# Kernel tuning notes

Measured on AMD Instinct MI355X. Metric: run time of the kernel, lower is better.

The kernel has to match this reference:

```python
import jax, jax.numpy as jnp
import numpy as np

N = 1024
IN_F = 256
OUT_F = 128
H = 4
NH = OUT_F // H  # 32
NEG_SLOPE = 0.2


def setup_inputs() -> dict:
    key = jax.random.key(0)
    k1, k2, k3, k4, k5 = jax.random.split(key, 5)
    h = jax.random.normal(k1, (N, IN_F), dtype=jnp.float32)
    adj_mat = jax.random.randint(k2, (N, N, 1), 0, 2, dtype=jnp.int32)
    s_in = 1.0 / np.sqrt(IN_F)
    s_nh = 1.0 / np.sqrt(NH)
    Wl = jax.random.uniform(k3, (H * NH, IN_F), jnp.float32, -s_in, s_in)
    Wr = jax.random.uniform(k4, (H * NH, IN_F), jnp.float32, -s_in, s_in)
    attn_w = jax.random.uniform(k5, (NH,), jnp.float32, -s_nh, s_nh)
    return {"h": h, "adj_mat": adj_mat, "Wl": Wl, "Wr": Wr, "attn_w": attn_w}


def reference(h, adj_mat, Wl, Wr, attn_w):
    n = h.shape[0]
    g_l = (h @ Wl.T).reshape(n, H, NH)  # [N,H,F]
    g_r = (h @ Wr.T).reshape(n, H, NH)  # [N,H,F]
    # g_sum[i, j] = g_l[j] + g_r[i]  (repeat / repeat_interleave semantics)
    g_sum = g_l[None, :, :, :] + g_r[:, None, :, :]  # [N,N,H,F]
    act = jnp.where(g_sum >= 0, g_sum, NEG_SLOPE * g_sum)
    e = jnp.einsum('ijhf,f->ijh', act, attn_w)  # [N,N,H]
    mask = adj_mat != 0  # [N,N,1] broadcasts over heads
    e = jnp.where(mask, e, -jnp.inf)
    a = jax.nn.softmax(e, axis=1)  # softmax over source nodes j
    h_prime = jnp.einsum('ijh,jhf->ihf', a, g_r).reshape(n, H * NH)
    # is_output_layer=False -> ELU (dropout is a no-op in eval)
    return jax.nn.elu(h_prime)
```

## Files before the change

kernel.cpp:

```cpp
#include <hip/hip_runtime.h>
#include <math.h>

#define NN 1024
#define IN_F 256
#define OUT_F 128
#define NHEADS 4
#define NHF 32
#define HPSTR 260

__global__ void __launch_bounds__(256) glr_gemm(const float* __restrict__ hmat,
                                                const float* __restrict__ Wl,
                                                const float* __restrict__ Wr,
                                                float* __restrict__ glh,
                                                float* __restrict__ grh) {
    __shared__ float hp[64 * HPSTR];
    const int tid = threadIdx.x;
    const int rg = blockIdx.x & 15;
    const int cs = blockIdx.x >> 4;

    const float4* __restrict__ hsrc = (const float4*)hmat + rg * (64 * 64);
#pragma unroll
    for (int i = 0; i < 16; ++i) {
        const int v = tid + i * 256;
        const int row = v >> 6, kq = v & 63;
        const float4 x = hsrc[v];
        *(float4*)(hp + row * HPSTR + kq * 4) = x;
    }
    __syncthreads();

    const int lane = tid & 63;
    const int wu = __builtin_amdgcn_readfirstlane(tid >> 6);
    const int c0 = cs * 16 + wu * 4;
    const float* __restrict__ wbase = (c0 < OUT_F) ? (Wl + c0 * IN_F)
                                                   : (Wr + (c0 - OUT_F) * IN_F);
    const float* __restrict__ hrow = hp + lane * HPSTR;

    float a0 = 0.f, a1 = 0.f, a2 = 0.f, a3 = 0.f;
#pragma unroll 4
    for (int kq = 0; kq < 64; ++kq) {
        const float4 hv = *(const float4*)(hrow + kq * 4);
        const float4 w0 = *(const float4*)(wbase + 0 * IN_F + kq * 4);
        const float4 w1 = *(const float4*)(wbase + 1 * IN_F + kq * 4);
        const float4 w2 = *(const float4*)(wbase + 2 * IN_F + kq * 4);
        const float4 w3 = *(const float4*)(wbase + 3 * IN_F + kq * 4);
        a0 = fmaf(hv.x, w0.x, fmaf(hv.y, w0.y, fmaf(hv.z, w0.z, fmaf(hv.w, w0.w, a0))));
        a1 = fmaf(hv.x, w1.x, fmaf(hv.y, w1.y, fmaf(hv.z, w1.z, fmaf(hv.w, w1.w, a1))));
        a2 = fmaf(hv.x, w2.x, fmaf(hv.y, w2.y, fmaf(hv.z, w2.z, fmaf(hv.w, w2.w, a2))));
        a3 = fmaf(hv.x, w3.x, fmaf(hv.y, w3.y, fmaf(hv.z, w3.z, fmaf(hv.w, w3.w, a3))));
    }

    const int row = rg * 64 + lane;
    const int cb = c0 & (OUT_F - 1);
    const int hh = cb >> 5;
    const int f  = cb & 31;
    float* __restrict__ dst = (c0 < OUT_F) ? glh : grh;
    float4 r; r.x = a0; r.y = a1; r.z = a2; r.w = a3;
    *(float4*)(dst + (hh * NN + row) * NHF + f) = r;
}

__global__ void __launch_bounds__(512) gat_main(const float* __restrict__ glh,
                                                const float* __restrict__ grh,
                                                const int* __restrict__ adj,
                                                const float* __restrict__ attn_w,
                                                float* __restrict__ out) {
    const int hh  = blockIdx.y;
    const int i0  = blockIdx.x * 8;
    const int tid = threadIdx.x;

    __shared__ float p_buf[8][1028];
    __shared__ float part[8][16][32];
    __shared__ float red[8][8];
    __shared__ float l_sh[8];

    float lpart[8];
#pragma unroll
    for (int ii = 0; ii < 8; ++ii) lpart[ii] = 0.f;

    for (int c = 0; c < 2; ++c) {
        const int j = (c << 9) + tid;
        const float* __restrict__ gp = glh + (hh * NN + j) * NHF;
        float gl[NHF];
#pragma unroll
        for (int f4 = 0; f4 < 8; ++f4) {
            const float4 v = *(const float4*)(gp + (f4 << 2));
            gl[4 * f4 + 0] = v.x; gl[4 * f4 + 1] = v.y;
            gl[4 * f4 + 2] = v.z; gl[4 * f4 + 3] = v.w;
        }
        float alpha = 0.f;
#pragma unroll
        for (int f = 0; f < NHF; ++f) alpha = fmaf(gl[f], attn_w[f], alpha);
        int adjv[8];
#pragma unroll
        for (int ii = 0; ii < 8; ++ii) adjv[ii] = adj[(i0 + ii) * NN + j];
#pragma unroll
        for (int ii = 0; ii < 8; ++ii) {
            const float* __restrict__ grp = grh + (hh * NN + i0 + ii) * NHF;
            float S0 = 0.f, S1 = 0.f;
#pragma unroll
            for (int f = 0; f < NHF; f += 2) {
                const float s0 = gl[f]     + grp[f];
                const float s1 = gl[f + 1] + grp[f + 1];
                S0 = fmaf(fabsf(s0), attn_w[f],     S0);
                S1 = fmaf(fabsf(s1), attn_w[f + 1], S1);
            }
            const float e = fmaf(0.4f, S0 + S1, 0.6f * alpha);
            const float p = adjv[ii] ? __expf(e) : 0.f;
            p_buf[ii][j] = p;
            lpart[ii] += p;
        }
    }

    const int lane = tid & 63, wv = tid >> 6;
#pragma unroll
    for (int ii = 0; ii < 8; ++ii) {
        float v = lpart[ii];
#pragma unroll
        for (int d = 32; d > 0; d >>= 1) v += __shfl_xor(v, d);
        if (lane == 0) red[ii][wv] = v;
    }
    __syncthreads();
    if (tid < 8) {
        float l = red[tid][0];
#pragma unroll
        for (int w = 1; w < 8; ++w) l += red[tid][w];
        l_sh[tid] = l;
    }
    __syncthreads();

    const int f  = tid & 31;
    const int js = tid >> 5;
    const float* __restrict__ gp = grh + hh * NN * NHF + f;
    float o[8];
#pragma unroll
    for (int ii = 0; ii < 8; ++ii) o[ii] = 0.f;
    const int jb = js << 6;
    for (int jj = 0; jj < 64; jj += 4) {
        const int j = jb + jj;
        const float g0 = gp[(j + 0) * NHF];
        const float g1 = gp[(j + 1) * NHF];
        const float g2 = gp[(j + 2) * NHF];
        const float g3 = gp[(j + 3) * NHF];
#pragma unroll
        for (int ii = 0; ii < 8; ++ii) {
            const float4 p4 = *(const float4*)&p_buf[ii][j];
            o[ii] = fmaf(p4.x, g0, fmaf(p4.y, g1, fmaf(p4.z, g2, fmaf(p4.w, g3, o[ii]))));
        }
    }
#pragma unroll
    for (int ii = 0; ii < 8; ++ii) part[ii][js][f] = o[ii];
    __syncthreads();

    if (tid < 256) {
        const int ii = tid >> 5, ff = tid & 31;
        float s = 0.f;
#pragma unroll
        for (int k = 0; k < 16; ++k) s += part[ii][k][ff];
        s /= l_sh[ii];
        const float r = (s > 0.f) ? s : (__expf(s) - 1.f);
        out[(i0 + ii) * OUT_F + hh * NHF + ff] = r;
    }
}

extern "C" void kernel_launch(void* const* d_in, const int* in_sizes, int n_in,
                              void* d_out, int out_size, void* d_ws, size_t ws_size,
                              hipStream_t stream) {
    const float* hmat = (const float*)d_in[0];
    const int*   adj  = (const int*)d_in[1];
    const float* Wl   = (const float*)d_in[2];
    const float* Wr   = (const float*)d_in[3];
    const float* aw   = (const float*)d_in[4];
    float* o          = (float*)d_out;

    float* glh = (float*)d_ws;
    float* grh = glh + NHEADS * NN * NHF;

    glr_gemm<<<dim3(256), dim3(256), 0, stream>>>(hmat, Wl, Wr, glh, grh);
    gat_main<<<dim3(NN / 8, NHEADS), dim3(512), 0, stream>>>(glh, grh, adj, aw, o);
}
```

Baseline: 101.0 us.

## Shrink row tiles and split GEMM K across lanes to raise parallelism

The projection GEMM now uses 16-row tiles with the K dimension split across four lane groups, reduced by shuffles, and launches four times as many blocks. The attention kernel processes 4 destination rows per block instead of 8, which doubles the grid. Its score loop now loads g_l in 16-wide halves to lower register pressure, and launch bounds are raised to encourage higher occupancy. The aim is to fill the GPU better and hide latency. The cost is that each adjacency and g_r column pass is amortized over fewer rows, so the repeated global loads per row grow.

After: 101.1 us. No clear change (+0.2%).

```diff
diff --git a/kernel.cpp b/kernel.cpp
--- a/kernel.cpp
+++ b/kernel.cpp
@@ -6,104 +6,122 @@
 #define OUT_F 128
 #define NHEADS 4
 #define NHF 32
+#define ITILE 4
 #define HPSTR 260
 
-__global__ void __launch_bounds__(256) glr_gemm(const float* __restrict__ hmat,
-                                                const float* __restrict__ Wl,
-                                                const float* __restrict__ Wr,
-                                                float* __restrict__ glh,
-                                                float* __restrict__ grh) {
-    __shared__ float hp[64 * HPSTR];
+__global__ void __launch_bounds__(256, 4) glr_gemm(const float* __restrict__ hmat,
+                                                   const float* __restrict__ Wl,
+                                                   const float* __restrict__ Wr,
+                                                   float* __restrict__ glh,
+                                                   float* __restrict__ grh) {
+    __shared__ float hp[16 * HPSTR];
     const int tid = threadIdx.x;
-    const int rg = blockIdx.x & 15;
-    const int cs = blockIdx.x >> 4;
-
-    const float4* __restrict__ hsrc = (const float4*)hmat + rg * (64 * 64);
-#pragma unroll
-    for (int i = 0; i < 16; ++i) {
+    const int rg = blockIdx.x & 63;
+    const int cs = blockIdx.x >> 6;
+
+    const float4* __restrict__ hsrc = (const float4*)hmat + rg * (16 * 64);
+#pragma unroll
+    for (int i = 0; i < 4; ++i) {
         const int v = tid + i * 256;
         const int row = v >> 6, kq = v & 63;
-        const float4 x = hsrc[v];
-        *(float4*)(hp + row * HPSTR + kq * 4) = x;
+        *(float4*)(hp + row * HPSTR + kq * 4) = hsrc[v];
     }
     __syncthreads();
 
     const int lane = tid & 63;
-    const int wu = __builtin_amdgcn_readfirstlane(tid >> 6);
-    const int c0 = cs * 16 + wu * 4;
-    const float* __restrict__ wbase = (c0 < OUT_F) ? (Wl + c0 * IN_F)
-                                                   : (Wr + (c0 - OUT_F) * IN_F);
-    const float* __restrict__ hrow = hp + lane * HPSTR;
+    const int row  = lane & 15;
+    const int kc   = lane >> 4;
+    const int wu   = __builtin_amdgcn_readfirstlane(tid >> 6);
+    const int c0   = cs * 16 + wu * 4;
+    const float* __restrict__ wb = (c0 < OUT_F) ? (Wl + c0 * IN_F)
+                                                : (Wr + (c0 - OUT_F) * IN_F);
+    const float* __restrict__ hrow = hp + row * HPSTR + kc * 64;
+    const float* __restrict__ wrow = wb + kc * 64;
 
     float a0 = 0.f, a1 = 0.f, a2 = 0.f, a3 = 0.f;
 #pragma unroll 4
-    for (int kq = 0; kq < 64; ++kq) {
-        const float4 hv = *(const float4*)(hrow + kq * 4);
-        const float4 w0 = *(const float4*)(wbase + 0 * IN_F + kq * 4);
-        const float4 w1 = *(const float4*)(wbase + 1 * IN_F + kq * 4);
-        const float4 w2 = *(const float4*)(wbase + 2 * IN_F + kq * 4);
-        const float4 w3 = *(const float4*)(wbase + 3 * IN_F + kq * 4);
+    for (int i = 0; i < 16; ++i) {
+        const float4 hv = *(const float4*)(hrow + i * 4);
+        const float4 w0 = *(const float4*)(wrow + 0 * IN_F + i * 4);
+        const float4 w1 = *(const float4*)(wrow + 1 * IN_F + i * 4);
+        const float4 w2 = *(const float4*)(wrow + 2 * IN_F + i * 4);
+        const float4 w3 = *(const float4*)(wrow + 3 * IN_F + i * 4);
         a0 = fmaf(hv.x, w0.x, fmaf(hv.y, w0.y, fmaf(hv.z, w0.z, fmaf(hv.w, w0.w, a0))));
         a1 = fmaf(hv.x, w1.x, fmaf(hv.y, w1.y, fmaf(hv.z, w1.z, fmaf(hv.w, w1.w, a1))));
         a2 = fmaf(hv.x, w2.x, fmaf(hv.y, w2.y, fmaf(hv.z, w2.z, fmaf(hv.w, w2.w, a2))));
         a3 = fmaf(hv.x, w3.x, fmaf(hv.y, w3.y, fmaf(hv.z, w3.z, fmaf(hv.w, w3.w, a3))));
     }
-
-    const int row = rg * 64 + lane;
-    const int cb = c0 & (OUT_F - 1);
-    const int hh = cb >> 5;
-    const int f  = cb & 31;
-    float* __restrict__ dst = (c0 < OUT_F) ? glh : grh;
-    float4 r; r.x = a0; r.y = a1; r.z = a2; r.w = a3;
-    *(float4*)(dst + (hh * NN + row) * NHF + f) = r;
+    a0 += __shfl_xor(a0, 16); a0 += __shfl_xor(a0, 32);
+    a1 += __shfl_xor(a1, 16); a1 += __shfl_xor(a1, 32);
+    a2 += __shfl_xor(a2, 16); a2 += __shfl_xor(a2, 32);
+    a3 += __shfl_xor(a3, 16); a3 += __shfl_xor(a3, 32);
+
+    if (kc == 0) {
+        const int cb = c0 & (OUT_F - 1);
+        const int hh = cb >> 5;
+        const int f  = cb & 31;
+        float* __restrict__ dst = (c0 < OUT_F) ? glh : grh;
+        float4 r; r.x = a0; r.y = a1; r.z = a2; r.w = a3;
+        *(float4*)(dst + (hh * NN + rg * 16 + row) * NHF + f) = r;
+    }
 }
 
-__global__ void __launch_bounds__(512) gat_main(const float* __restrict__ glh,
-                                                const float* __restrict__ grh,
-                                                const int* __restrict__ adj,
-                                                const float* __restrict__ attn_w,
-                                                float* __restrict__ out) {
+__global__ void __launch_bounds__(512, 8) gat_main(const float* __restrict__ glh,
+                                                   const float* __restrict__ grh,
+                                                   const int* __restrict__ adj,
+                                                   const float* __restrict__ attn_w,
+                                                   float* __restrict__ out) {
     const int hh  = blockIdx.y;
-    const int i0  = blockIdx.x * 8;
+    const int i0  = blockIdx.x * ITILE;
     const int tid = threadIdx.x;
 
-    __shared__ float p_buf[8][1028];
-    __shared__ float part[8][16][32];
-    __shared__ float red[8][8];
-    __shared__ float l_sh[8];
-
-    float lpart[8];
-#pragma unroll
-    for (int ii = 0; ii < 8; ++ii) lpart[ii] = 0.f;
-
+    __shared__ float p_buf[ITILE][1028];
+    __shared__ float part[ITILE][16][NHF];
+    __shared__ float red[ITILE][8];
+    __shared__ float l_sh[ITILE];
+
+    float lpart[ITILE];
+#pragma unroll
+    for (int ii = 0; ii < ITILE; ++ii) lpart[ii] = 0.f;
+
+#pragma unroll 1
     for (int c = 0; c < 2; ++c) {
         const int j = (c << 9) + tid;
         const float* __restrict__ gp = glh + (hh * NN + j) * NHF;
-        float gl[NHF];
-#pragma unroll
-        for (int f4 = 0; f4 < 8; ++f4) {
-            const float4 v = *(const float4*)(gp + (f4 << 2));
-            gl[4 * f4 + 0] = v.x; gl[4 * f4 + 1] = v.y;
-            gl[4 * f4 + 2] = v.z; gl[4 * f4 + 3] = v.w;
-        }
+        int adjv[ITILE];
+#pragma unroll
+        for (int ii = 0; ii < ITILE; ++ii) adjv[ii] = adj[(i0 + ii) * NN + j];
+
+        float S[ITILE];
+#pragma unroll
+        for (int ii = 0; ii < ITILE; ++ii) S[ii] = 0.f;
         float alpha = 0.f;
-#pragma unroll
-        for (int f = 0; f < NHF; ++f) alpha = fmaf(gl[f], attn_w[f], alpha);
-        int adjv[8];
-#pragma unroll
-        for (int ii = 0; ii < 8; ++ii) adjv[ii] = adj[(i0 + ii) * NN + j];
-#pragma unroll
-        for (int ii = 0; ii < 8; ++ii) {
-            const float* __restrict__ grp = grh + (hh * NN + i0 + ii) * NHF;
-            float S0 = 0.f, S1 = 0.f;
-#pragma unroll
-            for (int f = 0; f < NHF; f += 2) {
-                const float s0 = gl[f]     + grp[f];
-                const float s1 = gl[f + 1] + grp[f + 1];
-                S0 = fmaf(fabsf(s0), attn_w[f],     S0);
-                S1 = fmaf(fabsf(s1), attn_w[f + 1], S1);
+
+#pragma unroll
+        for (int fh = 0; fh < 2; ++fh) {
+            const int fb = fh << 4;
+            float g[16];
+#pragma unroll
+            for (int f4 = 0; f4 < 4; ++f4) {
+                const float4 v = *(const float4*)(gp + fb + (f4 << 2));
+                g[4 * f4 + 0] = v.x; g[4 * f4 + 1] = v.y;
+                g[4 * f4 + 2] = v.z; g[4 * f4 + 3] = v.w;
             }
-            const float e = fmaf(0.4f, S0 + S1, 0.6f * alpha);
+#pragma unroll
+            for (int k = 0; k < 16; ++k) alpha = fmaf(g[k], attn_w[fb + k], alpha);
+#pragma unroll
+            for (int ii = 0; ii < ITILE; ++ii) {
+                const float* __restrict__ grp = grh + (hh * NN + i0 + ii) * NHF + fb;
+                float s = S[ii];
+#pragma unroll
+                for (int k = 0; k < 16; ++k)
+                    s = fmaf(fabsf(g[k] + grp[k]), attn_w[fb + k], s);
+                S[ii] = s;
+            }
+        }
+#pragma unroll
+        for (int ii = 0; ii < ITILE; ++ii) {
+            const float e = fmaf(0.4f, S[ii], 0.6f * alpha);
             const float p = adjv[ii] ? __expf(e) : 0.f;
             p_buf[ii][j] = p;
             lpart[ii] += p;
@@ -112,14 +130,14 @@
 
     const int lane = tid & 63, wv = tid >> 6;
 #pragma unroll
-    for (int ii = 0; ii < 8; ++ii) {
+    for (int ii = 0; ii < ITILE; ++ii) {
         float v = lpart[ii];
 #pragma unroll
         for (int d = 32; d > 0; d >>= 1) v += __shfl_xor(v, d);
         if (lane == 0) red[ii][wv] = v;
     }
     __syncthreads();
-    if (tid < 8) {
+    if (tid < ITILE) {
         float l = red[tid][0];
 #pragma unroll
         for (int w = 1; w < 8; ++w) l += red[tid][w];
@@ -130,10 +148,11 @@
     const int f  = tid & 31;
     const int js = tid >> 5;
     const float* __restrict__ gp = grh + hh * NN * NHF + f;
-    float o[8];
-#pragma unroll
-    for (int ii = 0; ii < 8; ++ii) o[ii] = 0.f;
+    float o[ITILE];
+#pragma unroll
+    for (int ii = 0; ii < ITILE; ++ii) o[ii] = 0.f;
     const int jb = js << 6;
+#pragma unroll 4
     for (int jj = 0; jj < 64; jj += 4) {
         const int j = jb + jj;
         const float g0 = gp[(j + 0) * NHF];
@@ -141,21 +160,26 @@
         const float g2 = gp[(j + 2) * NHF];
         const float g3 = gp[(j + 3) * NHF];
 #pragma unroll
-        for (int ii = 0; ii < 8; ++ii) {
+        for (int ii = 0; ii < ITILE; ++ii) {
             const float4 p4 = *(const float4*)&p_buf[ii][j];
             o[ii] = fmaf(p4.x, g0, fmaf(p4.y, g1, fmaf(p4.z, g2, fmaf(p4.w, g3, o[ii]))));
         }
     }
 #pragma unroll
-    for (int ii = 0; ii < 8; ++ii) part[ii][js][f] = o[ii];
-    __syncthreads();
-
-    if (tid < 256) {
+    for (int ii = 0; ii < ITILE; ++ii) part[ii][js][f] = o[ii];
+    __syncthreads();
+
+    if (tid < 32 * ITILE) {
         const int ii = tid >> 5, ff = tid & 31;
-        float s = 0.f;
-#pragma unroll
-        for (int k = 0; k < 16; ++k) s += part[ii][k][ff];
-        s /= l_sh[ii];
+        float s0 = 0.f, s1 = 0.f, s2 = 0.f, s3 = 0.f;
+#pragma unroll
+        for (int k = 0; k < 16; k += 4) {
+            s0 += part[ii][k + 0][ff];
+            s1 += part[ii][k + 1][ff];
+            s2 += part[ii][k + 2][ff];
+            s3 += part[ii][k + 3][ff];
+        }
+        float s = ((s0 + s1) + (s2 + s3)) / l_sh[ii];
         const float r = (s > 0.f) ? s : (__expf(s) - 1.f);
         out[(i0 + ii) * OUT_F + hh * NHF + ff] = r;
     }
@@ -174,6 +198,6 @@
     float* glh = (float*)d_ws;
     float* grh = glh + NHEADS * NN * NHF;
 
-    glr_gemm<<<dim3(256), dim3(256), 0, stream>>>(hmat, Wl, Wr, glh, grh);
-    gat_main<<<dim3(NN / 8, NHEADS), dim3(512), 0, stream>>>(glh, grh, adj, aw, o);
+    glr_gemm<<<dim3(1024), dim3(256), 0, stream>>>(hmat, Wl, Wr, glh, grh);
+    gat_main<<<dim3(NN / ITILE, NHEADS), dim3(512), 0, stream>>>(glh, grh, adj, aw, o);
 }
```
